# Kernel optimization log

Hardware: AMD Instinct MI355X
Metric: run time of the kernel (lower is better)

## Reference

```python
import jax, jax.numpy as jnp
import numpy as np
import math

N_EMBD = 1024
N_HEAD = 16
HEAD_DIM = N_EMBD // N_HEAD
B, T = 2, 2048
LORA_RANK = 16      # 8-bit setting
LORA_SCALE = 32.0 / 16.0  # alpha / rank
QMIN, QMAX = 0.0, 255.0   # 8-bit asymmetric


def round_ste(x):
    return x + jax.lax.stop_gradient(jnp.round(x) - x)


def fake_quant(x, scale, zero_point):
    # LearnableFakeQuantize, asymmetric 8-bit, straight-through round
    q = jnp.clip(round_ste(x / scale + zero_point), QMIN, QMAX)
    return (q - zero_point) * scale


def lora_linear(x, w, b, la, lb):
    # base linear + LoRA path (dropout disabled / eval)
    return x @ w + b + LORA_SCALE * ((x @ la) @ lb)


def setup_inputs() -> dict:
    key = jax.random.key(0)
    ks = jax.random.split(key, 10)
    std = 0.02
    hidden_states = jax.random.normal(ks[0], (B, T, N_EMBD), dtype=jnp.float32)
    w_attn = jax.random.normal(ks[1], (N_EMBD, 3 * N_EMBD), dtype=jnp.float32) * std
    b_attn = jnp.zeros((3 * N_EMBD,), dtype=jnp.float32)
    la_attn = jax.random.normal(ks[2], (N_EMBD, LORA_RANK), dtype=jnp.float32) * std
    lb_attn = jnp.zeros((LORA_RANK, 3 * N_EMBD), dtype=jnp.float32)
    w_proj = jax.random.normal(ks[3], (N_EMBD, N_EMBD), dtype=jnp.float32) * std
    b_proj = jnp.zeros((N_EMBD,), dtype=jnp.float32)
    la_proj = jax.random.normal(ks[4], (N_EMBD, LORA_RANK), dtype=jnp.float32) * std
    lb_proj = jnp.zeros((LORA_RANK, N_EMBD), dtype=jnp.float32)
    kv_scale = jnp.asarray(0.05, dtype=jnp.float32)
    kv_zero_point = jnp.asarray(128.0, dtype=jnp.float32)
    return {
        'hidden_states': hidden_states,
        'w_attn': w_attn, 'b_attn': b_attn, 'la_attn': la_attn, 'lb_attn': lb_attn,
        'w_proj': w_proj, 'b_proj': b_proj, 'la_proj': la_proj, 'lb_proj': lb_proj,
        'kv_scale': kv_scale, 'kv_zero_point': kv_zero_point,
    }


def reference(hidden_states, w_attn, b_attn, la_attn, lb_attn,
              w_proj, b_proj, la_proj, lb_proj, kv_scale, kv_zero_point):
    Bn, Tn, C = hidden_states.shape
    qkv = lora_linear(hidden_states, w_attn, b_attn, la_attn, lb_attn)
    q, k, v = jnp.split(qkv, 3, axis=2)
    # [B, T, C] -> [B, H, T, D]
    def to_heads(x):
        return x.reshape(Bn, Tn, N_HEAD, HEAD_DIM).transpose(0, 2, 1, 3)
    q, k, v = to_heads(q), to_heads(k), to_heads(v)
    k = fake_quant(k, kv_scale, kv_zero_point)
    v = fake_quant(v, kv_scale, kv_zero_point)
    scores = jnp.einsum('bhqd,bhkd->bhqk', q, k) / math.sqrt(HEAD_DIM)
    causal = jnp.tril(jnp.ones((Tn, Tn), dtype=bool))
    scores = jnp.where(causal, scores, -jnp.inf)
    attn = jax.nn.softmax(scores, axis=-1)
    out = jnp.einsum('bhqk,bhkd->bhqd', attn, v)
    out = out.transpose(0, 2, 1, 3).reshape(Bn, Tn, C)
    return lora_linear(out, w_proj, b_proj, la_proj, lb_proj)
```

## Files before the change

### kernel.cpp

```cpp
#include <hip/hip_runtime.h>
#include <hip/hip_bf16.h>
#include <math.h>

#define N_EMBD   1024
#define N_HEAD   16
#define HEAD_DIM 64
#define BATCH    2
#define TSEQ     2048
#define RANK     16
#define LORA_SCALE 2.0f
#define M_TOTAL  (BATCH * TSEQ)
#define C3       (3 * N_EMBD)

typedef unsigned short ushort_t;
typedef __attribute__((ext_vector_type(8))) short bf16x8;
typedef __attribute__((ext_vector_type(4))) float f32x4;

__device__ __forceinline__ float fake_quant(float x, float scale, float zp) {
    float q = rintf(x / scale + zp);
    q = fminf(fmaxf(q, 0.0f), 255.0f);
    return (q - zp) * scale;
}

__device__ __forceinline__ ushort_t bf16bits(float f) {
    union { __hip_bfloat16 h; ushort_t u; } c;
    c.h = __float2bfloat16(f);
    return c.u;
}

__device__ __forceinline__ float bfraw2f(ushort_t u) {
    union { unsigned int i; float f; } c; c.i = ((unsigned int)u) << 16; return c.f;
}

__global__ void cvt_split_kernel(const float* __restrict__ in,
                                 __hip_bfloat16* __restrict__ hi,
                                 __hip_bfloat16* __restrict__ lo, int n4) {
    int i = blockIdx.x * 256 + threadIdx.x;
    if (i >= n4) return;
    float4 v = ((const float4*)in)[i];
    float vs[4] = {v.x, v.y, v.z, v.w};
    #pragma unroll
    for (int k = 0; k < 4; ++k) {
        __hip_bfloat16 h = __float2bfloat16(vs[k]);
        hi[i * 4 + k] = h;
        lo[i * 4 + k] = __float2bfloat16(vs[k] - __bfloat162float(h));
    }
}

__global__ void transpose_split_kernel(const float* __restrict__ in,
                                       __hip_bfloat16* __restrict__ hiT,
                                       __hip_bfloat16* __restrict__ loT,
                                       int R, int C) {
    __shared__ float tl[32][33];
    const int c0 = blockIdx.x * 32, r0 = blockIdx.y * 32;
    const int tx = threadIdx.x & 31, ty = threadIdx.x >> 5;
    for (int i = ty; i < 32; i += 8)
        tl[i][tx] = in[(size_t)(r0 + i) * C + c0 + tx];
    __syncthreads();
    for (int i = ty; i < 32; i += 8) {
        float v = tl[tx][i];
        __hip_bfloat16 h = __float2bfloat16(v);
        size_t o = (size_t)(c0 + i) * R + r0 + tx;
        hiT[o] = h;
        if (loT) loT[o] = __float2bfloat16(v - __bfloat162float(h));
    }
}

__global__ void vtrans_kernel(const ushort_t* __restrict__ Vb,
                              ushort_t* __restrict__ Vt) {
    __shared__ ushort_t tl[64][68];
    const int bh = blockIdx.x & 31, tt = blockIdx.x >> 5;
    const int tid = threadIdx.x;
    {
        const int t = tid >> 2, d0 = (tid & 3) * 16;
        const uint4 u = *(const uint4*)(Vb + ((size_t)bh * TSEQ + tt * 64 + t) * 64 + d0);
        *(uint4*)&tl[t][d0] = u;
        *(uint4*)&tl[t][d0 + 8] = *(const uint4*)(Vb + ((size_t)bh * TSEQ + tt * 64 + t) * 64 + d0 + 8);
    }
    __syncthreads();
    const int d = tid >> 2, t0 = (tid & 3) * 16;
    unsigned int wbuf[8];
    #pragma unroll
    for (int j = 0; j < 8; ++j)
        wbuf[j] = (unsigned int)tl[t0 + 2 * j][d] | ((unsigned int)tl[t0 + 2 * j + 1][d] << 16);
    ushort_t* dst = Vt + ((size_t)bh * 64 + d) * TSEQ + tt * 64 + t0;
    *(uint4*)dst       = make_uint4(wbuf[0], wbuf[1], wbuf[2], wbuf[3]);
    *(uint4*)(dst + 8) = make_uint4(wbuf[4], wbuf[5], wbuf[6], wbuf[7]);
}

__global__ void lora_t_part_kernel(const float* __restrict__ x,
                                   const float* __restrict__ la,
                                   float* __restrict__ tpart, int K) {
    __shared__ float Xs[16][64];
    const int tid = threadIdx.x;
    const int ty = tid >> 4, tx = tid & 15;
    const int row0 = blockIdx.x * 16;
    const int kbase = blockIdx.y * 256;
    float acc = 0.0f;
    for (int k0 = kbase; k0 < kbase + 256; k0 += 64) {
        int rr = tid >> 4, kk = (tid & 15) * 4;
        float4 v = *(const float4*)(x + (size_t)(row0 + rr) * K + k0 + kk);
        Xs[rr][kk] = v.x; Xs[rr][kk + 1] = v.y; Xs[rr][kk + 2] = v.z; Xs[rr][kk + 3] = v.w;
        __syncthreads();
        for (int k = 0; k < 64; ++k)
            acc += Xs[ty][k] * la[(size_t)(k0 + k) * RANK + tx];
        __syncthreads();
    }
    tpart[((size_t)blockIdx.y * M_TOTAL + row0 + ty) * RANK + tx] = acc;
}

__global__ void lora_t_part_bf16_kernel(const ushort_t* __restrict__ x,
                                        const float* __restrict__ la,
                                        float* __restrict__ tpart, int K) {
    __shared__ float Xs[16][64];
    const int tid = threadIdx.x;
    const int ty = tid >> 4, tx = tid & 15;
    const int row0 = blockIdx.x * 16;
    const int kbase = blockIdx.y * 256;
    float acc = 0.0f;
    for (int k0 = kbase; k0 < kbase + 256; k0 += 64) {
        int rr = tid >> 4, kk = (tid & 15) * 4;
        const ushort4 u = *(const ushort4*)(x + (size_t)(row0 + rr) * K + k0 + kk);
        Xs[rr][kk] = bfraw2f(u.x); Xs[rr][kk + 1] = bfraw2f(u.y);
        Xs[rr][kk + 2] = bfraw2f(u.z); Xs[rr][kk + 3] = bfraw2f(u.w);
        __syncthreads();
        for (int k = 0; k < 64; ++k)
            acc += Xs[ty][k] * la[(size_t)(k0 + k) * RANK + tx];
        __syncthreads();
    }
    tpart[((size_t)blockIdx.y * M_TOTAL + row0 + ty) * RANK + tx] = acc;
}

__device__ __forceinline__ int sw_off(int r, int c) {
    return ((r >> 1) << 7) + (((((r & 1) << 2) | c) ^ ((r >> 1) & 7)) << 4);
}

template <bool SPLIT>
__global__ __launch_bounds__(256, 3)
void gemm_mfma_kernel(const __hip_bfloat16* __restrict__ Ah,
                      const __hip_bfloat16* __restrict__ Al,
                      const __hip_bfloat16* __restrict__ Bh,
                      const __hip_bfloat16* __restrict__ Bl,
                      const float* __restrict__ bias,
                      const float* __restrict__ tpart,
                      const float* __restrict__ lb,
                      float* __restrict__ Cf,
                      ushort_t* __restrict__ Qb,
                      ushort_t* __restrict__ Kb,
                      ushort_t* __restrict__ Vb,
                      const float* __restrict__ sp,
                      const float* __restrict__ zp,
                      int M, int N, int K, int split_col0, int out_mode) {
    constexpr int TILE = 128 * 32;
    __shared__ __hip_bfloat16 As[(SPLIT ? 2 : 1) * TILE];
    __shared__ __hip_bfloat16 Bs[(SPLIT ? 2 : 1) * TILE];
    __shared__ float Ts[128 * 16];
    __shared__ float Ls[16 * 128];

    const int tid = threadIdx.x;
    const int lane = tid & 63, w = tid >> 6;

    int bcol, brow, phase;
    {
        const int NC = gridDim.x, NR = gridDim.y;
        const int lid = blockIdx.y * NC + blockIdx.x;
        const int xcd = lid & 7, s = lid >> 3;
        const int cw = NC >> 1, rh = NR >> 2;
        const int cg = xcd & 1, rg = xcd >> 1;
        if (SPLIT) {
            bcol = 2 * (s % cw) + cg;
            brow = rg * rh + (s / cw);
            phase = (lid * 7 + (s >> 5) * 11) & 31;
        } else {
            bcol = cg * cw + (s % cw);
            brow = rg * rh + (s / cw);
            phase = (lid * 7) & 31;
        }
    }
    const int row0 = brow * 128, col0 = bcol * 128;
    const int wr = (w >> 1) * 64, wc = (w & 1) * 64;
    const bool do_split = SPLIT && (col0 >= split_col0);

    const int s_lc = (lane & 7) ^ ((lane >> 3) & 7);
    const int s_rb = 2 * (lane >> 3) + (s_lc >> 2);
    const int s_c8 = (s_lc & 3) * 8;

    float qsc = 0.f, qzp = 0.f;
    if (out_mode == 1) { qsc = sp[0]; qzp = zp[0]; }

    f32x4 acc[4][4];
    #pragma unroll
    for (int i = 0; i < 4; ++i)
        #pragma unroll
        for (int j = 0; j < 4; ++j)
            acc[i][j] = (f32x4){0.f, 0.f, 0.f, 0.f};

    const int arow = wr + (lane & 15);
    const int chunk = lane >> 4;

    const int KI = K >> 5;
    for (int kk = 0; kk < KI; ++kk) {
        const int k0 = (((kk + phase) & (KI - 1)) << 5);
        #pragma unroll
        for (int qq = 0; qq < 2; ++qq) {
            const int q = 2 * w + qq;
            const int r = 16 * q + s_rb;
            const __hip_bfloat16* gA = Ah + (size_t)(row0 + r) * K + k0 + s_c8;
            __builtin_amdgcn_global_load_lds(
                (const __attribute__((address_space(1))) void*)gA,
                (__attribute__((address_space(3))) void*)(As + q * 512), 16, 0, 0);
            const __hip_bfloat16* gB = Bh + (size_t)(col0 + r) * K + k0 + s_c8;
            __builtin_amdgcn_global_load_lds(
                (const __attribute__((address_space(1))) void*)gB,
                (__attribute__((address_space(3))) void*)(Bs + q * 512), 16, 0, 0);
            if (do_split) {
                const __hip_bfloat16* gAl = Al + (size_t)(row0 + r) * K + k0 + s_c8;
                __builtin_amdgcn_global_load_lds(
                    (const __attribute__((address_space(1))) void*)gAl,
                    (__attribute__((address_space(3))) void*)(As + TILE + q * 512), 16, 0, 0);
                const __hip_bfloat16* gBl = Bl + (size_t)(col0 + r) * K + k0 + s_c8;
                __builtin_amdgcn_global_load_lds(
                    (const __attribute__((address_space(1))) void*)gBl,
                    (__attribute__((address_space(3))) void*)(Bs + TILE + q * 512), 16, 0, 0);
            }
        }
        __syncthreads();

        const char* ab = (const char*)As;
        const char* bb = (const char*)Bs;
        bf16x8 a_h[4], b_h[4], a_l[4], b_l[4];
        #pragma unroll
        for (int mi = 0; mi < 4; ++mi) {
            int off = sw_off(arow + mi * 16, chunk);
            a_h[mi] = *(const bf16x8*)(ab + off);
            if (do_split) a_l[mi] = *(const bf16x8*)(ab + 2 * TILE + off);
        }
        #pragma unroll
        for (int nj = 0; nj < 4; ++nj) {
            int off = sw_off(wc + nj * 16 + (lane & 15), chunk);
            b_h[nj] = *(const bf16x8*)(bb + off);
            if (do_split) b_l[nj] = *(const bf16x8*)(bb + 2 * TILE + off);
        }
        #pragma unroll
        for (int mi = 0; mi < 4; ++mi)
            #pragma unroll
            for (int nj = 0; nj < 4; ++nj) {
                acc[mi][nj] = __builtin_amdgcn_mfma_f32_16x16x32_bf16(a_h[mi], b_h[nj], acc[mi][nj], 0, 0, 0);
                if (do_split) {
                    acc[mi][nj] = __builtin_amdgcn_mfma_f32_16x16x32_bf16(a_h[mi], b_l[nj], acc[mi][nj], 0, 0, 0);
                    acc[mi][nj] = __builtin_amdgcn_mfma_f32_16x16x32_bf16(a_l[mi], b_h[nj], acc[mi][nj], 0, 0, 0);
                }
            }
        __syncthreads();
    }

    {
        int r = tid >> 1, j0 = (tid & 1) * 8;
        float4 t0 = {0, 0, 0, 0}, t1 = {0, 0, 0, 0};
        #pragma unroll
        for (int c = 0; c < 4; ++c) {
            const float* src = tpart + ((size_t)c * M_TOTAL + row0 + r) * RANK + j0;
            float4 s0 = *(const float4*)src;
            float4 s1 = *(const float4*)(src + 4);
            t0.x += s0.x; t0.y += s0.y; t0.z += s0.z; t0.w += s0.w;
            t1.x += s1.x; t1.y += s1.y; t1.z += s1.z; t1.w += s1.w;
        }
        *(float4*)(Ts + r * 16 + j0)     = t0;
        *(float4*)(Ts + r * 16 + j0 + 4) = t1;
        int rr = tid >> 4, c0 = (tid & 15) * 8;
        const float4* lsrc = (const float4*)(lb + (size_t)rr * N + col0 + c0);
        float4* ldst = (float4*)(Ls + rr * 128 + c0);
        ldst[0] = lsrc[0]; ldst[1] = lsrc[1];
    }
    __syncthreads();
    #pragma unroll
    for (int mi = 0; mi < 4; ++mi)
        #pragma unroll
        for (int nj = 0; nj < 4; ++nj) {
            const int coll = wc + nj * 16 + (lane & 15);
            const float bv = bias[col0 + coll];
            #pragma unroll
            for (int rg = 0; rg < 4; ++rg) {
                const int rowl = wr + mi * 16 + (lane >> 4) * 4 + rg;
                float lsum = 0.f;
                #pragma unroll
                for (int rr = 0; rr < 16; ++rr)
                    lsum += Ts[rowl * 16 + rr] * Ls[rr * 128 + coll];
                const float val = acc[mi][nj][rg] + bv + LORA_SCALE * lsum;
                if (out_mode == 0) {
                    Cf[(size_t)(row0 + rowl) * N + col0 + coll] = val;
                } else {
                    const int R = row0 + rowl;
                    const int b = R >> 11, t = R & 2047;
                    const int CN = col0 + coll;
                    const int sec = CN >> 10, head = (CN >> 6) & 15, d = CN & 63;
                    const size_t off = (((size_t)(b * 16 + head)) * TSEQ + t) * 64 + d;
                    if (sec == 0)      Qb[off] = bf16bits(val * 0.125f);
                    else if (sec == 1) Kb[off] = bf16bits(fake_quant(val, qsc, qzp));
                    else               Vb[off] = bf16bits(fake_quant(val, qsc, qzp));
                }
            }
        }
}

__global__ __launch_bounds__(256)
void mfma_attn_kernel(const ushort_t* __restrict__ Qb,
                      const ushort_t* __restrict__ Kq,
                      const ushort_t* __restrict__ Vtq,
                      ushort_t* __restrict__ outb) {
    const int bx = blockIdx.x;
    const int bh = bx & 31;
    const int qt = 31 - (bx >> 5);
    const int b = bh >> 4, h = bh & 15;
    const int tid = threadIdx.x;
    const int lane = tid & 63, w = tid >> 6;
    const int m16 = lane & 15, qc = lane >> 4;
    const int m7 = m16 & 7;

    __shared__ ushort_t Qs[4096];
    __shared__ ushort_t Ks[4096];
    __shared__ ushort_t Vs[4096];
    __shared__ ushort_t Ps[4096];

    const int s_g = (lane & 7) ^ ((lane >> 3) & 7);
    const int s_r = lane >> 3;

    const ushort_t* Qg = Qb + (size_t)bh * TSEQ * 64;
    const ushort_t* Kg = Kq + (size_t)bh * TSEQ * 64;
    const ushort_t* Vg = Vtq + (size_t)bh * 64 * TSEQ;

    #pragma unroll
    for (int pp = 0; pp < 2; ++pp) {
        const int p = 2 * w + pp;
        const ushort_t* gq = Qg + ((size_t)(qt * 64 + 8 * p + s_r)) * 64 + s_g * 8;
        __builtin_amdgcn_global_load_lds(
            (const __attribute__((address_space(1))) void*)gq,
            (__attribute__((address_space(3))) void*)(Qs + p * 512), 16, 0, 0);
    }
    __syncthreads();

    bf16x8 a_q[2];
    {
        const int row = 16 * w + m16;
        #pragma unroll
        for (int c = 0; c < 2; ++c) {
            const int g = qc + 4 * c;
            a_q[c] = *(const bf16x8*)((const char*)Qs + row * 128 + ((g ^ m7) << 4));
        }
    }

    float m_st[4], l_st[4];
    f32x4 o_acc[4];
    #pragma unroll
    for (int r = 0; r < 4; ++r) { m_st[r] = -INFINITY; l_st[r] = 0.0f; }
    #pragma unroll
    for (int dj = 0; dj < 4; ++dj) o_acc[dj] = (f32x4){0.f, 0.f, 0.f, 0.f};

    for (int kt = 0; kt <= qt; ++kt) {
        __syncthreads();
        #pragma unroll
        for (int pp = 0; pp < 2; ++pp) {
            const int p = 2 * w + pp;
            const ushort_t* gk = Kg + ((size_t)(kt * 64 + 8 * p + s_r)) * 64 + s_g * 8;
            __builtin_amdgcn_global_load_lds(
                (const __attribute__((address_space(1))) void*)gk,
                (__attribute__((address_space(3))) void*)(Ks + p * 512), 16, 0, 0);
            const ushort_t* gv = Vg + ((size_t)(8 * p + s_r)) * TSEQ + kt * 64 + s_g * 8;
            __builtin_amdgcn_global_load_lds(
                (const __attribute__((address_space(1))) void*)gv,
                (__attribute__((address_space(3))) void*)(Vs + p * 512), 16, 0, 0);
        }
        __syncthreads();

        const bool diag = (kt == qt);
        const int nj_hi = diag ? (w + 1) : 4;

        f32x4 s[4];
        #pragma unroll
        for (int nj = 0; nj < 4; ++nj) s[nj] = (f32x4){0.f, 0.f, 0.f, 0.f};
        #pragma unroll
        for (int c = 0; c < 2; ++c) {
            #pragma unroll
            for (int nj = 0; nj < 4; ++nj) {
                if (nj < nj_hi) {
                    const int row = 16 * nj + m16;
                    const int g = qc + 4 * c;
                    bf16x8 bk = *(const bf16x8*)((const char*)Ks + row * 128 + ((g ^ m7) << 4));
                    s[nj] = __builtin_amdgcn_mfma_f32_16x16x32_bf16(a_q[c], bk, s[nj], 0, 0, 0);
                }
            }
        }

        float alpha[4], p_[4][4];
        #pragma unroll
        for (int reg = 0; reg < 4; ++reg) {
            const int qrow = 16 * w + 4 * qc + reg;
            float sv[4];
            float rm = -INFINITY;
            #pragma unroll
            for (int nj = 0; nj < 4; ++nj) {
                float v = s[nj][reg];
                if (diag && (m16 + 16 * nj > qrow)) v = -INFINITY;
                sv[nj] = v;
                rm = fmaxf(rm, v);
            }
            #pragma unroll
            for (int off = 1; off < 16; off <<= 1)
                rm = fmaxf(rm, __shfl_xor(rm, off, 16));
            const float mo = m_st[reg];
            const float mn = fmaxf(mo, rm);
            const float al = __expf(mo - mn);
            float rs = 0.f;
            #pragma unroll
            for (int nj = 0; nj < 4; ++nj) {
                float pv = __expf(sv[nj] - mn);
                p_[reg][nj] = pv;
                rs += pv;
            }
            #pragma unroll
            for (int off = 1; off < 16; off <<= 1)
                rs += __shfl_xor(rs, off, 16);
            l_st[reg] = al * l_st[reg] + rs;
            m_st[reg] = mn;
            alpha[reg] = al;
        }

        #pragma unroll
        for (int reg = 0; reg < 4; ++reg) {
            const int row = 16 * w + 4 * qc + reg;
            const int r7 = row & 7;
            #pragma unroll
            for (int nj = 0; nj < 4; ++nj) {
                const int k = m16 + 16 * nj;
                Ps[row * 64 + (((k >> 3) ^ r7) << 3) + (k & 7)] = bf16bits(p_[reg][nj]);
            }
        }

        #pragma unroll
        for (int dj = 0; dj < 4; ++dj)
            #pragma unroll
            for (int reg = 0; reg < 4; ++reg)
                o_acc[dj][reg] *= alpha[reg];

        const int c_hi = diag ? (w >= 2 ? 2 : 1) : 2;
        #pragma unroll
        for (int c = 0; c < 2; ++c) {
            if (c < c_hi) {
                const int rowp = 16 * w + m16;
                const int g = qc + 4 * c;
                bf16x8 ap = *(const bf16x8*)((const char*)Ps + rowp * 128 + ((g ^ m7) << 4));
                #pragma unroll
                for (int dj = 0; dj < 4; ++dj) {
                    const int rowv = 16 * dj + m16;
                    bf16x8 bv = *(const bf16x8*)((const char*)Vs + rowv * 128 + ((g ^ m7) << 4));
                    o_acc[dj] = __builtin_amdgcn_mfma_f32_16x16x32_bf16(ap, bv, o_acc[dj], 0, 0, 0);
                }
            }
        }
    }

    #pragma unroll
    for (int reg = 0; reg < 4; ++reg) {
        const float inv = 1.0f / l_st[reg];
        const int q = qt * 64 + 16 * w + 4 * qc + reg;
        #pragma unroll
        for (int dj = 0; dj < 4; ++dj) {
            const int d = m16 + 16 * dj;
            outb[((size_t)b * TSEQ + q) * N_EMBD + h * 64 + d] = bf16bits(o_acc[dj][reg] * inv);
        }
    }
}

extern "C" void kernel_launch(void* const* d_in, const int* in_sizes, int n_in,
                              void* d_out, int out_size, void* d_ws, size_t ws_size,
                              hipStream_t stream) {
    const float* x        = (const float*)d_in[0];
    const float* w_attn   = (const float*)d_in[1];
    const float* b_attn   = (const float*)d_in[2];
    const float* la_attn  = (const float*)d_in[3];
    const float* lb_attn  = (const float*)d_in[4];
    const float* w_proj   = (const float*)d_in[5];
    const float* b_proj   = (const float*)d_in[6];
    const float* la_proj  = (const float*)d_in[7];
    const float* lb_proj  = (const float*)d_in[8];
    const float* kv_scale = (const float*)d_in[9];
    const float* kv_zp    = (const float*)d_in[10];
    float* out = (float*)d_out;

    char* ws = (char*)d_ws;
    float* t_attn_p       = (float*)ws;          ws += (size_t)4 * M_TOTAL * RANK * 4;
    float* t_proj_p       = (float*)ws;          ws += (size_t)4 * M_TOTAL * RANK * 4;
    ushort_t* aob         = (ushort_t*)ws;       ws += (size_t)M_TOTAL * N_EMBD * 2;
    __hip_bfloat16* x_hi  = (__hip_bfloat16*)ws; ws += (size_t)M_TOTAL * N_EMBD * 2;
    __hip_bfloat16* x_lo  = (__hip_bfloat16*)ws; ws += (size_t)M_TOTAL * N_EMBD * 2;
    __hip_bfloat16* wqT_h = (__hip_bfloat16*)ws; ws += (size_t)C3 * N_EMBD * 2;
    __hip_bfloat16* wqT_l = (__hip_bfloat16*)ws; ws += (size_t)C3 * N_EMBD * 2;
    __hip_bfloat16* wpT   = (__hip_bfloat16*)ws; ws += (size_t)N_EMBD * N_EMBD * 2;
    ushort_t* Qb          = (ushort_t*)ws;       ws += (size_t)32 * TSEQ * 64 * 2;
    ushort_t* Kb          = (ushort_t*)ws;       ws += (size_t)32 * TSEQ * 64 * 2;
    ushort_t* Vb          = (ushort_t*)ws;       ws += (size_t)32 * TSEQ * 64 * 2;
    ushort_t* Vtq         = (ushort_t*)ws;       ws += (size_t)32 * 64 * TSEQ * 2;

    cvt_split_kernel<<<dim3(M_TOTAL * N_EMBD / 4 / 256), 256, 0, stream>>>(
        x, x_hi, x_lo, M_TOTAL * N_EMBD / 4);
    transpose_split_kernel<<<dim3(C3 / 32, N_EMBD / 32), 256, 0, stream>>>(
        w_attn, wqT_h, wqT_l, N_EMBD, C3);
    transpose_split_kernel<<<dim3(N_EMBD / 32, N_EMBD / 32), 256, 0, stream>>>(
        w_proj, wpT, nullptr, N_EMBD, N_EMBD);
    lora_t_part_kernel<<<dim3(M_TOTAL / 16, 4), 256, 0, stream>>>(x, la_attn, t_attn_p, N_EMBD);

    gemm_mfma_kernel<true><<<dim3(24, 32), 256, 0, stream>>>(
        x_hi, x_lo, wqT_h, wqT_l, b_attn, t_attn_p, lb_attn,
        nullptr, Qb, Kb, Vb, kv_scale, kv_zp,
        M_TOTAL, C3, N_EMBD, 2 * N_EMBD, 1);

    vtrans_kernel<<<dim3(32 * (TSEQ / 64)), 256, 0, stream>>>(Vb, Vtq);

    mfma_attn_kernel<<<dim3(32 * 32), 256, 0, stream>>>(Qb, Kb, Vtq, aob);

    lora_t_part_bf16_kernel<<<dim3(M_TOTAL / 16, 4), 256, 0, stream>>>(aob, la_proj, t_proj_p, N_EMBD);

    gemm_mfma_kernel<false><<<dim3(8, 32), 256, 0, stream>>>(
        (const __hip_bfloat16*)aob, nullptr, wpT, nullptr, b_proj, t_proj_p, lb_proj,
        out, nullptr, nullptr, nullptr, nullptr, nullptr,
        M_TOTAL, N_EMBD, N_EMBD, 1 << 30, 0);
}
```

Measured before the change: 348.4 us.

## Double-buffer LDS tiles in GEMM and attention to overlap loads with MFMA

Both the GEMM and the attention kernel now use ping-pong LDS buffers. The next K-slice or KV tile is issued via global_load_lds while MFMAs run on the current buffer, which hides global-load latency and removes one barrier per iteration in attention. The GEMM drops its per-block K-phase rotation and aliases the LoRA scratch (Ts/Ls) onto the staging buffers. The split variant's launch bound is lowered to 2 blocks per CU because LDS doubles. Larger LDS use may cut occupancy, and the aliasing relies on correct barriers around the epilogue.

```diff
diff --git a/kernel.cpp b/kernel.cpp
--- a/kernel.cpp
+++ b/kernel.cpp
@@ -136,7 +136,7 @@
 }
 
 template <bool SPLIT>
-__global__ __launch_bounds__(256, 3)
+__global__ __launch_bounds__(256, SPLIT ? 2 : 3)
 void gemm_mfma_kernel(const __hip_bfloat16* __restrict__ Ah,
                       const __hip_bfloat16* __restrict__ Al,
                       const __hip_bfloat16* __restrict__ Bh,
@@ -152,15 +152,16 @@
                       const float* __restrict__ zp,
                       int M, int N, int K, int split_col0, int out_mode) {
     constexpr int TILE = 128 * 32;
-    __shared__ __hip_bfloat16 As[(SPLIT ? 2 : 1) * TILE];
-    __shared__ __hip_bfloat16 Bs[(SPLIT ? 2 : 1) * TILE];
-    __shared__ float Ts[128 * 16];
-    __shared__ float Ls[16 * 128];
+    constexpr int BUFE = (SPLIT ? 2 : 1) * TILE;
+    __shared__ __align__(16) __hip_bfloat16 As[2 * BUFE];
+    __shared__ __align__(16) __hip_bfloat16 Bs[2 * BUFE];
+    float* Ts = (float*)As;
+    float* Ls = (float*)Bs;
 
     const int tid = threadIdx.x;
     const int lane = tid & 63, w = tid >> 6;
 
-    int bcol, brow, phase;
+    int bcol, brow;
     {
         const int NC = gridDim.x, NR = gridDim.y;
         const int lid = blockIdx.y * NC + blockIdx.x;
@@ -170,11 +171,9 @@
         if (SPLIT) {
             bcol = 2 * (s % cw) + cg;
             brow = rg * rh + (s / cw);
-            phase = (lid * 7 + (s >> 5) * 11) & 31;
         } else {
             bcol = cg * cw + (s % cw);
             brow = rg * rh + (s / cw);
-            phase = (lid * 7) & 31;
         }
     }
     const int row0 = brow * 128, col0 = bcol * 128;
@@ -198,9 +197,10 @@
     const int arow = wr + (lane & 15);
     const int chunk = lane >> 4;
 
-    const int KI = K >> 5;
-    for (int kk = 0; kk < KI; ++kk) {
-        const int k0 = (((kk + phase) & (KI - 1)) << 5);
+    auto stage = [&](int buf, int kidx) {
+        const int k0 = kidx << 5;
+        __hip_bfloat16* dA = As + buf * BUFE;
+        __hip_bfloat16* dB = Bs + buf * BUFE;
         #pragma unroll
         for (int qq = 0; qq < 2; ++qq) {
             const int q = 2 * w + qq;
@@ -208,26 +208,33 @@
             const __hip_bfloat16* gA = Ah + (size_t)(row0 + r) * K + k0 + s_c8;
             __builtin_amdgcn_global_load_lds(
                 (const __attribute__((address_space(1))) void*)gA,
-                (__attribute__((address_space(3))) void*)(As + q * 512), 16, 0, 0);
+                (__attribute__((address_space(3))) void*)(dA + q * 512), 16, 0, 0);
             const __hip_bfloat16* gB = Bh + (size_t)(col0 + r) * K + k0 + s_c8;
             __builtin_amdgcn_global_load_lds(
                 (const __attribute__((address_space(1))) void*)gB,
-                (__attribute__((address_space(3))) void*)(Bs + q * 512), 16, 0, 0);
+                (__attribute__((address_space(3))) void*)(Bs + buf * BUFE + q * 512), 16, 0, 0);
             if (do_split) {
                 const __hip_bfloat16* gAl = Al + (size_t)(row0 + r) * K + k0 + s_c8;
                 __builtin_amdgcn_global_load_lds(
                     (const __attribute__((address_space(1))) void*)gAl,
-                    (__attribute__((address_space(3))) void*)(As + TILE + q * 512), 16, 0, 0);
+                    (__attribute__((address_space(3))) void*)(dA + TILE + q * 512), 16, 0, 0);
                 const __hip_bfloat16* gBl = Bl + (size_t)(col0 + r) * K + k0 + s_c8;
                 __builtin_amdgcn_global_load_lds(
                     (const __attribute__((address_space(1))) void*)gBl,
-                    (__attribute__((address_space(3))) void*)(Bs + TILE + q * 512), 16, 0, 0);
-            }
-        }
-        __syncthreads();
-
-        const char* ab = (const char*)As;
-        const char* bb = (const char*)Bs;
+                    (__attribute__((address_space(3))) void*)(dB + TILE + q * 512), 16, 0, 0);
+            }
+        }
+    };
+
+    const int KI = K >> 5;
+    stage(0, 0);
+    __syncthreads();
+    for (int kk = 0; kk < KI; ++kk) {
+        const int cur = kk & 1;
+        if (kk + 1 < KI) stage(cur ^ 1, kk + 1);
+
+        const char* ab = (const char*)(As + cur * BUFE);
+        const char* bb = (const char*)(Bs + cur * BUFE);
         bf16x8 a_h[4], b_h[4], a_l[4], b_l[4];
         #pragma unroll
         for (int mi = 0; mi < 4; ++mi) {
@@ -318,8 +325,8 @@
     const int m7 = m16 & 7;
 
     __shared__ ushort_t Qs[4096];
-    __shared__ ushort_t Ks[4096];
-    __shared__ ushort_t Vs[4096];
+    __shared__ ushort_t Ks[2][4096];
+    __shared__ ushort_t Vs[2][4096];
     __shared__ ushort_t Ps[4096];
 
     const int s_g = (lane & 7) ^ ((lane >> 3) & 7);
@@ -328,6 +335,21 @@
     const ushort_t* Qg = Qb + (size_t)bh * TSEQ * 64;
     const ushort_t* Kg = Kq + (size_t)bh * TSEQ * 64;
     const ushort_t* Vg = Vtq + (size_t)bh * 64 * TSEQ;
+
+    auto stageKV = [&](int buf, int kt) {
+        #pragma unroll
+        for (int pp = 0; pp < 2; ++pp) {
+            const int p = 2 * w + pp;
+            const ushort_t* gk = Kg + ((size_t)(kt * 64 + 8 * p + s_r)) * 64 + s_g * 8;
+            __builtin_amdgcn_global_load_lds(
+                (const __attribute__((address_space(1))) void*)gk,
+                (__attribute__((address_space(3))) void*)(Ks[buf] + p * 512), 16, 0, 0);
+            const ushort_t* gv = Vg + ((size_t)(8 * p + s_r)) * TSEQ + kt * 64 + s_g * 8;
+            __builtin_amdgcn_global_load_lds(
+                (const __attribute__((address_space(1))) void*)gv,
+                (__attribute__((address_space(3))) void*)(Vs[buf] + p * 512), 16, 0, 0);
+        }
+    };
 
     #pragma unroll
     for (int pp = 0; pp < 2; ++pp) {
@@ -337,6 +359,7 @@
             (const __attribute__((address_space(1))) void*)gq,
             (__attribute__((address_space(3))) void*)(Qs + p * 512), 16, 0, 0);
     }
+    stageKV(0, 0);
     __syncthreads();
 
     bf16x8 a_q[2];
@@ -357,20 +380,8 @@
     for (int dj = 0; dj < 4; ++dj) o_acc[dj] = (f32x4){0.f, 0.f, 0.f, 0.f};
 
     for (int kt = 0; kt <= qt; ++kt) {
-        __syncthreads();
-        #pragma unroll
-        for (int pp = 0; pp < 2; ++pp) {
-            const int p = 2 * w + pp;
-            const ushort_t* gk = Kg + ((size_t)(kt * 64 + 8 * p + s_r)) * 64 + s_g * 8;
-            __builtin_amdgcn_global_load_lds(
-                (const __attribute__((address_space(1))) void*)gk,
-                (__attribute__((address_space(3))) void*)(Ks + p * 512), 16, 0, 0);
-            const ushort_t* gv = Vg + ((size_t)(8 * p + s_r)) * TSEQ + kt * 64 + s_g * 8;
-            __builtin_amdgcn_global_load_lds(
-                (const __attribute__((address_space(1))) void*)gv,
-                (__attribute__((address_space(3))) void*)(Vs + p * 512), 16, 0, 0);
-        }
-        __syncthreads();
+        const int cur = kt & 1;
+        if (kt < qt) stageKV(cur ^ 1, kt + 1);
 
         const bool diag = (kt == qt);
         const int nj_hi = diag ? (w + 1) : 4;
@@ -385,7 +396,7 @@
                 if (nj < nj_hi) {
                     const int row = 16 * nj + m16;
                     const int g = qc + 4 * c;
-                    bf16x8 bk = *(const bf16x8*)((const char*)Ks + row * 128 + ((g ^ m7) << 4));
+                    bf16x8 bk = *(const bf16x8*)((const char*)Ks[cur] + row * 128 + ((g ^ m7) << 4));
                     s[nj] = __builtin_amdgcn_mfma_f32_16x16x32_bf16(a_q[c], bk, s[nj], 0, 0, 0);
                 }
             }
@@ -452,11 +463,12 @@
                 #pragma unroll
                 for (int dj = 0; dj < 4; ++dj) {
                     const int rowv = 16 * dj + m16;
-                    bf16x8 bv = *(const bf16x8*)((const char*)Vs + rowv * 128 + ((g ^ m7) << 4));
+                    bf16x8 bv = *(const bf16x8*)((const char*)Vs[cur] + rowv * 128 + ((g ^ m7) << 4));
                     o_acc[dj] = __builtin_amdgcn_mfma_f32_16x16x32_bf16(ap, bv, o_acc[dj], 0, 0, 0);
                 }
             }
         }
+        __syncthreads();
     }
 
     #pragma unroll
```

Measured after the change: 356.9 us. +2.4%, slower.
